# Optimization experiments

Measured on AMD Instinct MI355X. Metric: run time of the kernel, lower is better.

Reference implementation:

```python
import jax, jax.numpy as jnp
import numpy as np

C = 2048
N = 8
K = C // N  # 256
B = 4096


def setup_inputs() -> dict:
    key = jax.random.key(0)
    ks = jax.random.split(key, 9)
    s_in = 1.0 / np.sqrt(C)
    s_k = 1.0 / np.sqrt(K)
    return {
        "x": jax.random.normal(ks[0], (B, C), dtype=jnp.float32),
        # weights stored [in, out] (y = x @ W + b), equivalent to torch Linear
        "W_theta": jax.random.uniform(ks[1], (C, K), jnp.float32, -s_in, s_in),
        "b_theta": jax.random.uniform(ks[2], (K,), jnp.float32, -s_in, s_in),
        "W_phi": jax.random.uniform(ks[3], (C, K), jnp.float32, -s_in, s_in),
        "b_phi": jax.random.uniform(ks[4], (K,), jnp.float32, -s_in, s_in),
        "W_f": jax.random.uniform(ks[5], (C, K), jnp.float32, -s_in, s_in),
        "b_f": jax.random.uniform(ks[6], (K,), jnp.float32, -s_in, s_in),
        "W_g": jax.random.uniform(ks[7], (K, C), jnp.float32, -s_k, s_k),
        "b_g": jax.random.uniform(ks[8], (C,), jnp.float32, -s_k, s_k),
    }


def reference(x, W_theta, b_theta, W_phi, b_phi, W_f, b_f, W_g, b_g):
    theta = x @ W_theta + b_theta          # [B, K]
    phi = x @ W_phi + b_phi                # [B, K]
    f = x @ W_f + b_f                      # [B, K]
    # outer product per sample -> [B, K, K], softmax over last dim
    scores = jax.nn.softmax(theta[:, :, None] * phi[:, None, :], axis=-1)
    t = jnp.einsum('bij,bj->bi', scores, f)  # [B, K]
    return x + t @ W_g + b_g               # residual, [B, C]
```

## Files before the change

### kernel.cpp

```cpp
#include <hip/hip_runtime.h>

constexpr int Bsz   = 4096;
constexpr int Cdim  = 2048;
constexpr int Kdim  = 256;
constexpr int PROJW = 3 * Kdim;
constexpr int KSPLIT = 4;

typedef __attribute__((ext_vector_type(8))) short short8;
typedef __attribute__((ext_vector_type(4))) float floatx4;
typedef __attribute__((ext_vector_type(2))) float float2v;
typedef __attribute__((ext_vector_type(4))) _Float16 half4v;

__device__ __forceinline__ unsigned short f2bf(float f) {
    unsigned int u = __float_as_uint(f);
    u += 0x7FFFu + ((u >> 16) & 1u);
    return (unsigned short)(u >> 16);
}

__device__ __forceinline__ void load16(const void* g, void* lds) {
    __builtin_amdgcn_global_load_lds(
        (const __attribute__((address_space(1))) unsigned int*)g,
        (__attribute__((address_space(3))) unsigned int*)lds, 16, 0, 0);
}


__global__ __launch_bounds__(256) void prep_kernel(
    const float* __restrict__ x, unsigned short* __restrict__ xb2,
    const float* __restrict__ Wt, const float* __restrict__ Wp,
    const float* __restrict__ Wf, const float* __restrict__ Wg,
    unsigned short* __restrict__ Wcat2, unsigned short* __restrict__ WgT)
{
    __shared__ float tile[32][33];
    const int bid = blockIdx.x;
    if (bid < 8192) {
        const int i   = bid * 256 + threadIdx.x;
        const int row = i >> 9;
        const int kq  = i & 511;
        float4 v = reinterpret_cast<const float4*>(x)[i];
        ushort4 o;
        o.x = f2bf(v.x); o.y = f2bf(v.y); o.z = f2bf(v.z); o.w = f2bf(v.w);
        const size_t dst = ((size_t)(row >> 7) * 64 + (kq >> 3)) * 4096 +
                           (row & 127) * 32 + (kq & 7) * 4;
        *reinterpret_cast<ushort4*>(xb2 + dst) = o;
        return;
    }
    const int q = bid - 8192;
    const int z = q >> 9;
    const int tileId = q & 511;
    const float* __restrict__ in;
    int R, C;
    if (z < 3) {
        in = (z == 0) ? Wt : (z == 1) ? Wp : Wf;
        R = Cdim; C = Kdim;
    } else {
        in = Wg; R = Kdim; C = Cdim;
    }
    const int ctiles = C / 32;
    const int c0 = (tileId % ctiles) * 32;
    const int r0 = (tileId / ctiles) * 32;
    const int tx = threadIdx.x & 31, ty = threadIdx.x >> 5;
#pragma unroll
    for (int i = ty; i < 32; i += 8)
        tile[i][tx] = in[(size_t)(r0 + i) * C + c0 + tx];
    __syncthreads();
    if (z < 3) {
#pragma unroll
        for (int i = ty; i < 32; i += 8) {
            const int cg = z * 256 + c0 + i;
            Wcat2[((size_t)(cg >> 7) * 64 + (r0 >> 5)) * 4096 +
                  (cg & 127) * 32 + tx] = f2bf(tile[tx][i]);
        }
    } else {
#pragma unroll
        for (int i = ty; i < 32; i += 8)
            WgT[(size_t)(c0 + i) * R + r0 + tx] = f2bf(tile[tx][i]);
    }
}

constexpr int RPS = 152;

__global__ __launch_bounds__(256) void proj_mfma(
    const unsigned short* __restrict__ xb2,
    const unsigned short* __restrict__ Wcat2,
    _Float16* __restrict__ pp)
{
    __shared__ __align__(16) char pool[128 * RPS * 2];
    short* As = (short*)pool;
    short* Bs = As + 128 * 32;

    const int tid  = threadIdx.x;
    const int lane = tid & 63;
    const int wid  = tid >> 6;
    const int wr   = wid >> 1, wc = wid & 1;

    const int L    = blockIdx.x;
    const int xcd  = L & 7;
    const int slot = L >> 3;
    const int rowTile = xcd * 4 + slot / 6;
    const int colTile = slot % 6;
    const int rowBase = rowTile * 128;
    const int colBase = colTile * 128;
    const int kz      = blockIdx.y;

    floatx4 acc[4][4] = {};

    const unsigned short* gA =
        xb2 + ((size_t)rowTile * 64 + kz * 16) * 4096 + tid * 8;
    const unsigned short* gB =
        Wcat2 + ((size_t)colTile * 64 + kz * 16) * 4096 + tid * 8;

    short* ldsA0 = As + ((tid & ~63)) * 8;
    short* ldsA1 = As + (256 + (tid & ~63)) * 8;
    short* ldsB0 = Bs + ((tid & ~63)) * 8;
    short* ldsB1 = Bs + (256 + (tid & ~63)) * 8;

    const int mrow = lane & 15;
    const int kgrp = lane >> 4;

    for (int kt = 0; kt < 16; ++kt) {
        load16(gA, ldsA0); load16(gA + 2048, ldsA1);
        load16(gB, ldsB0); load16(gB + 2048, ldsB1);
        gA += 4096; gB += 4096;
        __syncthreads();

        short8 af[4], bfr[4];
#pragma unroll
        for (int i = 0; i < 4; ++i)
            af[i]  = *(const short8*)&As[(wr * 64 + i * 16 + mrow) * 32 + kgrp * 8];
#pragma unroll
        for (int j = 0; j < 4; ++j)
            bfr[j] = *(const short8*)&Bs[(wc * 64 + j * 16 + mrow) * 32 + kgrp * 8];
#pragma unroll
        for (int i = 0; i < 4; ++i)
#pragma unroll
            for (int j = 0; j < 4; ++j)
                acc[i][j] = __builtin_amdgcn_mfma_f32_16x16x32_bf16(
                    af[i], bfr[j], acc[i][j], 0, 0, 0);
        __syncthreads();
    }

    _Float16* rp = (_Float16*)pool;
#pragma unroll
    for (int j = 0; j < 4; ++j) {
        const int cL = wc * 64 + j * 16 + mrow;
#pragma unroll
        for (int i = 0; i < 4; ++i)
#pragma unroll
            for (int r = 0; r < 4; ++r)
                rp[(wr * 64 + i * 16 + kgrp * 4 + r) * RPS + cL] =
                    (_Float16)acc[i][j][r];
    }
    __syncthreads();

    _Float16* __restrict__ dst = pp + (size_t)kz * Bsz * PROJW;
#pragma unroll
    for (int it = 0; it < 8; ++it) {
        const int c    = it * 256 + tid;
        const int rowL = c >> 4;
        const int ch   = c & 15;
        const float4 v = *reinterpret_cast<const float4*>(&rp[rowL * RPS + ch * 8]);
        *reinterpret_cast<float4*>(
            &dst[(size_t)(rowBase + rowL) * PROJW + colBase + ch * 8]) = v;
    }
}

__global__ __launch_bounds__(256) void attn_kernel(
    const _Float16* __restrict__ pp,
    const float* __restrict__ bt, const float* __restrict__ bp,
    const float* __restrict__ bff,
    unsigned short* __restrict__ t)
{
    __shared__ float sphi[4][Kdim];
    __shared__ float sff[4][Kdim];

    const int tid = threadIdx.x;
    const int s   = tid >> 6;
    const int l   = tid & 63;
    const int b   = blockIdx.x * 4 + s;
    const int j0  = l * 4;
    const size_t rowOff = (size_t)b * PROJW;

    float4 th = *reinterpret_cast<const float4*>(bt + j0);
    float4 ph = *reinterpret_cast<const float4*>(bp + j0);
    float4 fv = *reinterpret_cast<const float4*>(bff + j0);
#pragma unroll
    for (int z = 0; z < KSPLIT; ++z) {
        const _Float16* __restrict__ r = pp + (size_t)z * Bsz * PROJW + rowOff;
        half4v a = *reinterpret_cast<const half4v*>(r + j0);
        half4v c = *reinterpret_cast<const half4v*>(r + Kdim + j0);
        half4v d = *reinterpret_cast<const half4v*>(r + 2 * Kdim + j0);
        th.x += (float)a.x; th.y += (float)a.y; th.z += (float)a.z; th.w += (float)a.w;
        ph.x += (float)c.x; ph.y += (float)c.y; ph.z += (float)c.z; ph.w += (float)c.w;
        fv.x += (float)d.x; fv.y += (float)d.y; fv.z += (float)d.z; fv.w += (float)d.w;
    }
    const float tl[4] = {th.x * 1.44269504f, th.y * 1.44269504f,
                         th.z * 1.44269504f, th.w * 1.44269504f};
    *reinterpret_cast<float4*>(&sphi[s][j0]) = ph;
    *reinterpret_cast<float4*>(&sff[s][j0])  = fv;
    __syncthreads();

    float2v sa[4][2] = {}, na[4][2] = {};
    const float4* __restrict__ sp  = reinterpret_cast<const float4*>(sphi[s]);
    const float4* __restrict__ sfp = reinterpret_cast<const float4*>(sff[s]);
#pragma unroll 4
    for (int p = 0; p < Kdim / 4; ++p) {
        const float4 ph4 = sp[p];
        const float4 ff4 = sfp[p];
        const float2v p01 = {ph4.x, ph4.y};
        const float2v p23 = {ph4.z, ph4.w};
        const float2v f01 = {ff4.x, ff4.y};
        const float2v f23 = {ff4.z, ff4.w};
#pragma unroll
        for (int i = 0; i < 4; ++i) {
            const float2v a01 = tl[i] * p01;
            const float2v a23 = tl[i] * p23;
            float2v e01, e23;
            e01.x = __builtin_amdgcn_exp2f(a01.x);
            e01.y = __builtin_amdgcn_exp2f(a01.y);
            e23.x = __builtin_amdgcn_exp2f(a23.x);
            e23.y = __builtin_amdgcn_exp2f(a23.y);
            sa[i][0] += e01;
            sa[i][1] += e23;
            na[i][0] += e01 * f01;
            na[i][1] += e23 * f23;
        }
    }
    ushort4 o;
    unsigned short* op = &o.x;
#pragma unroll
    for (int i = 0; i < 4; ++i) {
        const float den = sa[i][0].x + sa[i][0].y + sa[i][1].x + sa[i][1].y;
        const float num = na[i][0].x + na[i][0].y + na[i][1].x + na[i][1].y;
        op[i] = f2bf(num * __builtin_amdgcn_rcpf(den));
    }
    *reinterpret_cast<ushort4*>(t + (size_t)b * Kdim + j0) = o;
}

constexpr int OPS = 68;

__global__ __launch_bounds__(256) void out_mfma(
    const unsigned short* __restrict__ tb,
    const unsigned short* __restrict__ WgT,
    const float* __restrict__ bg,
    const float* __restrict__ x,
    float* __restrict__ out)
{
    __shared__ __align__(16) char pool[128 * OPS * 4];
    short* As = (short*)pool;
    short* Bs = As + 128 * 32;

    const int tid  = threadIdx.x;
    const int lane = tid & 63;
    const int wid  = tid >> 6;
    const int wr   = wid >> 1, wc = wid & 1;
    const int rowBase = blockIdx.x * 128;
    const int colBase = blockIdx.y * 128;

    floatx4 acc[4][4] = {};

    const unsigned short* gA0 = tb  + (size_t)(rowBase + (tid >> 2)) * Kdim + (tid & 3) * 8;
    const unsigned short* gA1 = tb  + (size_t)(rowBase + 64 + (tid >> 2)) * Kdim + (tid & 3) * 8;
    const unsigned short* gB0 = WgT + (size_t)(colBase + (tid >> 2)) * Kdim + (tid & 3) * 8;
    const unsigned short* gB1 = WgT + (size_t)(colBase + 64 + (tid >> 2)) * Kdim + (tid & 3) * 8;

    short* ldsA0 = As + ((tid & ~63)) * 8;
    short* ldsA1 = As + (256 + (tid & ~63)) * 8;
    short* ldsB0 = Bs + ((tid & ~63)) * 8;
    short* ldsB1 = Bs + (256 + (tid & ~63)) * 8;

    const int mrow = lane & 15;
    const int kgrp = lane >> 4;

    for (int kt = 0; kt < Kdim; kt += 32) {
        load16(gA0, ldsA0); load16(gA1, ldsA1);
        load16(gB0, ldsB0); load16(gB1, ldsB1);
        gA0 += 32; gA1 += 32; gB0 += 32; gB1 += 32;
        __syncthreads();

        short8 af[4], bfr[4];
#pragma unroll
        for (int i = 0; i < 4; ++i)
            af[i]  = *(const short8*)&As[(wr * 64 + i * 16 + mrow) * 32 + kgrp * 8];
#pragma unroll
        for (int j = 0; j < 4; ++j)
            bfr[j] = *(const short8*)&Bs[(wc * 64 + j * 16 + mrow) * 32 + kgrp * 8];
#pragma unroll
        for (int i = 0; i < 4; ++i)
#pragma unroll
            for (int j = 0; j < 4; ++j)
                acc[i][j] = __builtin_amdgcn_mfma_f32_16x16x32_bf16(
                    af[i], bfr[j], acc[i][j], 0, 0, 0);
        __syncthreads();
    }

    float* rp = (float*)pool;
#pragma unroll
    for (int h = 0; h < 2; ++h) {
        if (wc == h) {
#pragma unroll
            for (int j = 0; j < 4; ++j) {
                const int cL = j * 16 + mrow;
#pragma unroll
                for (int i = 0; i < 4; ++i)
#pragma unroll
                    for (int r = 0; r < 4; ++r)
                        rp[(wr * 64 + i * 16 + kgrp * 4 + r) * OPS + cL] =
                            acc[i][j][r];
            }
        }
        __syncthreads();
#pragma unroll
        for (int it = 0; it < 8; ++it) {
            const int c    = it * 256 + tid;
            const int rowL = c >> 4;
            const int ch   = c & 15;
            const float4 v = *reinterpret_cast<const float4*>(&rp[rowL * OPS + ch * 4]);
            const int colG = colBase + h * 64 + ch * 4;
            const size_t g = (size_t)(rowBase + rowL) * Cdim + colG;
            const float4 bgv = *reinterpret_cast<const float4*>(bg + colG);
            const float4 xv  = *reinterpret_cast<const float4*>(x + g);
            float4 o;
            o.x = v.x + bgv.x + xv.x;
            o.y = v.y + bgv.y + xv.y;
            o.z = v.z + bgv.z + xv.z;
            o.w = v.w + bgv.w + xv.w;
            *reinterpret_cast<float4*>(out + g) = o;
        }
        __syncthreads();
    }
}

extern "C" void kernel_launch(void* const* d_in, const int* in_sizes, int n_in,
                              void* d_out, int out_size, void* d_ws, size_t ws_size,
                              hipStream_t stream) {
    const float* x  = (const float*)d_in[0];
    const float* Wt = (const float*)d_in[1];
    const float* bt = (const float*)d_in[2];
    const float* Wp = (const float*)d_in[3];
    const float* bp = (const float*)d_in[4];
    const float* Wf = (const float*)d_in[5];
    const float* bf = (const float*)d_in[6];
    const float* Wg = (const float*)d_in[7];
    const float* bg = (const float*)d_in[8];
    float* out = (float*)d_out;

    char* w = (char*)d_ws;
    _Float16*       pp    = (_Float16*)w;
    unsigned short* xb2   = (unsigned short*)(w + 25165824);
    unsigned short* Wcat2 = (unsigned short*)(w + 41943040);
    unsigned short* WgT   = (unsigned short*)(w + 45088768);
    unsigned short* tb    = (unsigned short*)(w + 46137344);

    prep_kernel<<<10240, 256, 0, stream>>>(x, xb2, Wt, Wp, Wf, Wg, Wcat2, WgT);
    proj_mfma<<<dim3(192, KSPLIT), 256, 0, stream>>>(xb2, Wcat2, pp);
    attn_kernel<<<Bsz / 4, 256, 0, stream>>>(pp, bt, bp, bf, tb);
    out_mfma<<<dim3(Bsz / 128, Cdim / 128), 256, 0, stream>>>(tb, WgT, bg, x, out);
}
```

Baseline: 165.5 us.

## Double-buffer LDS in both GEMM kernels and widen x bf16 conversion

Both bf16 MFMA GEMM kernels now use double-buffered LDS tiles. The next K-slice is fetched with global_load_lds while MFMAs run on the current one, and each iteration needs one barrier instead of two. The x conversion in the prep kernel now has each thread handle 8 floats with a 16-byte store, which halves the block count. The LDS pool already held enough space for both buffers. The aim is to hide global load latency behind compute, at the cost of a manual vmcnt wait before each barrier.

```diff
diff --git a/kernel.cpp b/kernel.cpp
--- a/kernel.cpp
+++ b/kernel.cpp
@@ -32,19 +32,24 @@
 {
     __shared__ float tile[32][33];
     const int bid = blockIdx.x;
-    if (bid < 8192) {
+    if (bid < 4096) {
         const int i   = bid * 256 + threadIdx.x;
-        const int row = i >> 9;
-        const int kq  = i & 511;
-        float4 v = reinterpret_cast<const float4*>(x)[i];
-        ushort4 o;
-        o.x = f2bf(v.x); o.y = f2bf(v.y); o.z = f2bf(v.z); o.w = f2bf(v.w);
-        const size_t dst = ((size_t)(row >> 7) * 64 + (kq >> 3)) * 4096 +
-                           (row & 127) * 32 + (kq & 7) * 4;
-        *reinterpret_cast<ushort4*>(xb2 + dst) = o;
+        const int row = i >> 8;
+        const int kg  = i & 255;
+        const float4* xv = reinterpret_cast<const float4*>(x);
+        const float4 v0 = xv[2 * i];
+        const float4 v1 = xv[2 * i + 1];
+        short8 o;
+        o[0] = (short)f2bf(v0.x); o[1] = (short)f2bf(v0.y);
+        o[2] = (short)f2bf(v0.z); o[3] = (short)f2bf(v0.w);
+        o[4] = (short)f2bf(v1.x); o[5] = (short)f2bf(v1.y);
+        o[6] = (short)f2bf(v1.z); o[7] = (short)f2bf(v1.w);
+        const size_t dst = ((size_t)(row >> 7) * 64 + (kg >> 2)) * 4096 +
+                           (row & 127) * 32 + (kg & 3) * 8;
+        *reinterpret_cast<short8*>(xb2 + dst) = o;
         return;
     }
-    const int q = bid - 8192;
+    const int q = bid - 4096;
     const int z = q >> 9;
     const int tileId = q & 511;
     const float* __restrict__ in;
@@ -85,8 +90,7 @@
     _Float16* __restrict__ pp)
 {
     __shared__ __align__(16) char pool[128 * RPS * 2];
-    short* As = (short*)pool;
-    short* Bs = As + 128 * 32;
+    short* S = (short*)pool;
 
     const int tid  = threadIdx.x;
     const int lane = tid & 63;
@@ -109,34 +113,45 @@
     const unsigned short* gB =
         Wcat2 + ((size_t)colTile * 64 + kz * 16) * 4096 + tid * 8;
 
-    short* ldsA0 = As + ((tid & ~63)) * 8;
-    short* ldsA1 = As + (256 + (tid & ~63)) * 8;
-    short* ldsB0 = Bs + ((tid & ~63)) * 8;
-    short* ldsB1 = Bs + (256 + (tid & ~63)) * 8;
-
+    const int wbase = (tid & ~63) * 8;
     const int mrow = lane & 15;
     const int kgrp = lane >> 4;
 
+    load16(gA, S + wbase);        load16(gA + 2048, S + wbase + 2048);
+    load16(gB, S + 8192 + wbase); load16(gB + 2048, S + 8192 + wbase + 2048);
+    gA += 4096; gB += 4096;
+    asm volatile("s_waitcnt vmcnt(0)" ::: "memory");
+    __builtin_amdgcn_s_barrier();
+    asm volatile("" ::: "memory");
+
+    int cur = 0;
     for (int kt = 0; kt < 16; ++kt) {
-        load16(gA, ldsA0); load16(gA + 2048, ldsA1);
-        load16(gB, ldsB0); load16(gB + 2048, ldsB1);
-        gA += 4096; gB += 4096;
-        __syncthreads();
-
+        if (kt < 15) {
+            short* An = S + (cur ^ 1) * 4096;
+            short* Bn = S + 8192 + (cur ^ 1) * 4096;
+            load16(gA, An + wbase);        load16(gA + 2048, An + wbase + 2048);
+            load16(gB, Bn + wbase);        load16(gB + 2048, Bn + wbase + 2048);
+            gA += 4096; gB += 4096;
+        }
+        const short* Ac = S + cur * 4096;
+        const short* Bc = S + 8192 + cur * 4096;
         short8 af[4], bfr[4];
 #pragma unroll
         for (int i = 0; i < 4; ++i)
-            af[i]  = *(const short8*)&As[(wr * 64 + i * 16 + mrow) * 32 + kgrp * 8];
+            af[i]  = *(const short8*)&Ac[(wr * 64 + i * 16 + mrow) * 32 + kgrp * 8];
 #pragma unroll
         for (int j = 0; j < 4; ++j)
-            bfr[j] = *(const short8*)&Bs[(wc * 64 + j * 16 + mrow) * 32 + kgrp * 8];
+            bfr[j] = *(const short8*)&Bc[(wc * 64 + j * 16 + mrow) * 32 + kgrp * 8];
 #pragma unroll
         for (int i = 0; i < 4; ++i)
 #pragma unroll
             for (int j = 0; j < 4; ++j)
                 acc[i][j] = __builtin_amdgcn_mfma_f32_16x16x32_bf16(
                     af[i], bfr[j], acc[i][j], 0, 0, 0);
-        __syncthreads();
+        asm volatile("s_waitcnt vmcnt(0)" ::: "memory");
+        __builtin_amdgcn_s_barrier();
+        asm volatile("" ::: "memory");
+        cur ^= 1;
     }
 
     _Float16* rp = (_Float16*)pool;
@@ -246,8 +261,7 @@
     float* __restrict__ out)
 {
     __shared__ __align__(16) char pool[128 * OPS * 4];
-    short* As = (short*)pool;
-    short* Bs = As + 128 * 32;
+    short* S = (short*)pool;
 
     const int tid  = threadIdx.x;
     const int lane = tid & 63;
@@ -263,34 +277,45 @@
     const unsigned short* gB0 = WgT + (size_t)(colBase + (tid >> 2)) * Kdim + (tid & 3) * 8;
     const unsigned short* gB1 = WgT + (size_t)(colBase + 64 + (tid >> 2)) * Kdim + (tid & 3) * 8;
 
-    short* ldsA0 = As + ((tid & ~63)) * 8;
-    short* ldsA1 = As + (256 + (tid & ~63)) * 8;
-    short* ldsB0 = Bs + ((tid & ~63)) * 8;
-    short* ldsB1 = Bs + (256 + (tid & ~63)) * 8;
-
+    const int wbase = (tid & ~63) * 8;
     const int mrow = lane & 15;
     const int kgrp = lane >> 4;
 
-    for (int kt = 0; kt < Kdim; kt += 32) {
-        load16(gA0, ldsA0); load16(gA1, ldsA1);
-        load16(gB0, ldsB0); load16(gB1, ldsB1);
-        gA0 += 32; gA1 += 32; gB0 += 32; gB1 += 32;
-        __syncthreads();
-
+    load16(gA0, S + wbase);        load16(gA1, S + wbase + 2048);
+    load16(gB0, S + 8192 + wbase); load16(gB1, S + 8192 + wbase + 2048);
+    gA0 += 32; gA1 += 32; gB0 += 32; gB1 += 32;
+    asm volatile("s_waitcnt vmcnt(0)" ::: "memory");
+    __builtin_amdgcn_s_barrier();
+    asm volatile("" ::: "memory");
+
+    int cur = 0;
+    for (int kt = 0; kt < 8; ++kt) {
+        if (kt < 7) {
+            short* An = S + (cur ^ 1) * 4096;
+            short* Bn = S + 8192 + (cur ^ 1) * 4096;
+            load16(gA0, An + wbase);        load16(gA1, An + wbase + 2048);
+            load16(gB0, Bn + wbase);        load16(gB1, Bn + wbase + 2048);
+            gA0 += 32; gA1 += 32; gB0 += 32; gB1 += 32;
+        }
+        const short* Ac = S + cur * 4096;
+        const short* Bc = S + 8192 + cur * 4096;
         short8 af[4], bfr[4];
 #pragma unroll
         for (int i = 0; i < 4; ++i)
-            af[i]  = *(const short8*)&As[(wr * 64 + i * 16 + mrow) * 32 + kgrp * 8];
+            af[i]  = *(const short8*)&Ac[(wr * 64 + i * 16 + mrow) * 32 + kgrp * 8];
 #pragma unroll
         for (int j = 0; j < 4; ++j)
-            bfr[j] = *(const short8*)&Bs[(wc * 64 + j * 16 + mrow) * 32 + kgrp * 8];
+            bfr[j] = *(const short8*)&Bc[(wc * 64 + j * 16 + mrow) * 32 + kgrp * 8];
 #pragma unroll
         for (int i = 0; i < 4; ++i)
 #pragma unroll
             for (int j = 0; j < 4; ++j)
                 acc[i][j] = __builtin_amdgcn_mfma_f32_16x16x32_bf16(
                     af[i], bfr[j], acc[i][j], 0, 0, 0);
-        __syncthreads();
+        asm volatile("s_waitcnt vmcnt(0)" ::: "memory");
+        __builtin_amdgcn_s_barrier();
+        asm volatile("" ::: "memory");
+        cur ^= 1;
     }
 
     float* rp = (float*)pool;
@@ -351,7 +376,7 @@
     unsigned short* WgT   = (unsigned short*)(w + 45088768);
     unsigned short* tb    = (unsigned short*)(w + 46137344);
 
-    prep_kernel<<<10240, 256, 0, stream>>>(x, xb2, Wt, Wp, Wf, Wg, Wcat2, WgT);
+    prep_kernel<<<6144, 256, 0, stream>>>(x, xb2, Wt, Wp, Wf, Wg, Wcat2, WgT);
     proj_mfma<<<dim3(192, KSPLIT), 256, 0, stream>>>(xb2, Wcat2, pp);
     attn_kernel<<<Bsz / 4, 256, 0, stream>>>(pp, bt, bp, bf, tb);
     out_mfma<<<dim3(Bsz / 128, Cdim / 128), 256, 0, stream>>>(tb, WgT, bg, x, out);
```

After: 164.3 us. About the same (-0.8%).
